# Kernel tuning notes

Hardware: AMD Instinct MI355X
Metric: run time of the kernel (lower is better)

The kernel has to match this reference:

```python
import jax, jax.numpy as jnp
import numpy as np

IN_DIMS = [3, 16, 16]
OUT_DIMS = [16, 16, 3]
GRID_SIZE = 8
SPLINE_ORDER = 3
GRID_RANGE = (-1.0, 1.0)
K = GRID_SIZE + SPLINE_ORDER  # number of B-spline basis functions = 11

# extended knot grid, identical for every feature (as in standard KAN layers)
_h = (GRID_RANGE[1] - GRID_RANGE[0]) / GRID_SIZE
GRID_NP = np.arange(-SPLINE_ORDER, GRID_SIZE + SPLINE_ORDER + 1, dtype=np.float32) * _h + GRID_RANGE[0]

# per-layer parameter slice boundaries: [coef, univariate_weight, residual_weight] per layer
_sizes = [0]
for di, do in zip(IN_DIMS, OUT_DIMS):
    _sizes.extend([di * do * K, di * do, di * do])
PARAM_IDX = np.cumsum(_sizes)
KAN_PARAMS_NUM = int(PARAM_IDX[-1])  # 4576


def bspline_basis(x, grid):
    """Cox-de Boor recursion. x: [...,], grid: [G]. Returns [..., K]."""
    x = x[..., None]
    b = ((x >= grid[:-1]) & (x < grid[1:])).astype(x.dtype)
    for p in range(1, SPLINE_ORDER + 1):
        left = (x - grid[:-(p + 1)]) / (grid[p:-1] - grid[:-(p + 1)]) * b[..., :-1]
        right = (grid[p + 1:] - x) / (grid[p + 1:] - grid[1:-p]) * b[..., 1:]
        b = left + right
    return b  # [..., GRID_SIZE + SPLINE_ORDER]


def setup_inputs() -> dict:
    key = jax.random.key(0)
    k1, k2, k3, k4 = jax.random.split(key, 4)
    B, C, H, W = 8, 3, 224, 224
    x = jax.random.uniform(k1, (B, C, H, W), dtype=jnp.float32)  # in grid range
    features = jax.random.normal(k2, (B, 1000), dtype=jnp.float32)  # resnet18 output stand-in
    fc_w = jax.random.normal(k3, (KAN_PARAMS_NUM, 1000), dtype=jnp.float32) * 0.02
    fc_b = jax.random.normal(k4, (KAN_PARAMS_NUM,), dtype=jnp.float32) * 0.02
    return {"x": x, "features": features, "fc_w": fc_w, "fc_b": fc_b}


def reference(x, features, fc_w, fc_b):
    B, C, H, W = x.shape
    # hypernetwork head: per-sample flat KAN parameter vector [B, P]
    w = features @ fc_w.T + fc_b
    # image -> per-pixel tokens [B, T, C]
    y = jnp.transpose(x, (0, 2, 3, 1)).reshape(B, H * W, C)
    grid = jnp.asarray(GRID_NP, dtype=x.dtype)
    for n, (di, do) in enumerate(zip(IN_DIMS, OUT_DIMS)):
        i0, i1, i2, i3 = PARAM_IDX[3 * n: 3 * n + 4]
        coef = w[:, i0:i1].reshape(B, di, do, K)       # spline coefficients
        uw = w[:, i1:i2].reshape(B, di, do)            # univariate (spline) weight
        rw = w[:, i2:i3].reshape(B, di, do)            # residual (silu) weight
        basis = bspline_basis(y, grid)                 # [B, T, di, K]
        spline = jnp.einsum('btik,biok->bto', basis, coef * uw[..., None])
        base = jnp.einsum('bti,bio->bto', jax.nn.silu(y), rw)
        y = spline + base                              # [B, T, do]
    out = y.reshape(B, H, W, -1)
    return jnp.transpose(out, (0, 3, 1, 2))
```

## Files before the change

### kernel.cpp

```cpp
#include <hip/hip_runtime.h>

#define HW   50176
#define NPAR 4576

typedef _Float16 half8 __attribute__((ext_vector_type(8)));
typedef __attribute__((ext_vector_type(4))) float f32x4;
typedef __attribute__((ext_vector_type(4))) int int4v;

__device__ __forceinline__ unsigned short f2h(float f) {
    union { _Float16 h; unsigned short u; } c; c.h = (_Float16)f; return c.u;
}
__device__ __forceinline__ float h2f(unsigned short u) {
    union { _Float16 h; unsigned short u; } c; c.u = u; return (float)c.h;
}

__global__ __launch_bounds__(256) void gemm_w(const float* __restrict__ feats,
                                              const float* __restrict__ fcw,
                                              const float* __restrict__ fcb,
                                              float* __restrict__ wout) {
    __shared__ float red[4][64][4];
    int tid = threadIdx.x, lane = tid & 63, wave = tid >> 6;
    int nn = lane & 15, quad = lane >> 4;
    int n = blockIdx.x * 16 + nn;
    const float* brow = fcw + (size_t)n * 1000;
    const float* arow = feats + nn * 1000;

    f32x4 acc = {0.f, 0.f, 0.f, 0.f};
#pragma unroll 4
    for (int s8 = 0; s8 < 8; s8++) {
        int kb = (wave * 8 + s8) * 32 + quad * 8;
        float4 a0 = {0,0,0,0}, a1 = {0,0,0,0}, b0 = {0,0,0,0}, b1 = {0,0,0,0};
        if (kb < 1000) {
            b0 = *(const float4*)(brow + kb);
            b1 = *(const float4*)(brow + kb + 4);
            if (nn < 8) {
                a0 = *(const float4*)(arow + kb);
                a1 = *(const float4*)(arow + kb + 4);
            }
        }
        float af[8] = {a0.x, a0.y, a0.z, a0.w, a1.x, a1.y, a1.z, a1.w};
        float bf[8] = {b0.x, b0.y, b0.z, b0.w, b1.x, b1.y, b1.z, b1.w};
        half8 ah, al, bh;
#pragma unroll
        for (int j = 0; j < 8; j++) {
            ah[j] = (_Float16)af[j];
            al[j] = (_Float16)(af[j] - (float)ah[j]);
            bh[j] = (_Float16)bf[j];
        }
        acc = __builtin_amdgcn_mfma_f32_16x16x32_f16(ah, bh, acc, 0, 0, 0);
        acc = __builtin_amdgcn_mfma_f32_16x16x32_f16(al, bh, acc, 0, 0, 0);
    }
#pragma unroll
    for (int r = 0; r < 4; r++) red[wave][lane][r] = acc[r];
    __syncthreads();
    if (wave == 0 && quad < 2) {
        float bias = fcb[n];
#pragma unroll
        for (int r = 0; r < 4; r++) {
            float v = red[0][lane][r] + red[1][lane][r]
                    + red[2][lane][r] + red[3][lane][r];
            wout[(size_t)(quad * 4 + r) * NPAR + n] = v + bias;
        }
    }
}

__global__ __launch_bounds__(256) void pack_b(const float* __restrict__ w,
                                              unsigned int* __restrict__ bt) {
    int idx = blockIdx.x * 256 + threadIdx.x;
    if (idx >= 8 * 4608) return;
    int b = idx / 4608, r = idx - b * 4608;
    int ks = r >> 8, ln = (r >> 2) & 63, dq = r & 3;
    int q = ln >> 4, n = ln & 15;
    int lay, s;
    if (ks < 2)       { lay = 0; s = ks; }
    else if (ks < 10) { lay = 1; s = ks - 2; }
    else              { lay = 2; s = ks - 10; }
    int i = 2 * s + (q >> 1);
    const float* wb = w + b * NPAR;
    int cb, ub, rb2, nd, ni;
    if (lay == 0)      { cb = 0;    ub = 528;  rb2 = 576;  nd = 16; ni = 3;  }
    else if (lay == 1) { cb = 624;  ub = 3440; rb2 = 3696; nd = 16; ni = 16; }
    else               { cb = 3952; ub = 4480; rb2 = 4528; nd = 3;  ni = 16; }
    unsigned int pk = 0;
    if (i < ni && n < nd) {
        float uwv = wb[ub + i * nd + n];
        float rwv = wb[rb2 + i * nd + n];
        unsigned short rh = f2h(rwv);
        float rl = rwv - h2f(rh);
#pragma unroll
        for (int h = 0; h < 2; h++) {
            int rk = (q & 1) * 8 + dq * 2 + h;
            float v = 0.f;
            if (rk < 11)       v = wb[cb + (i * nd + n) * 11 + rk] * uwv;
            else if (rk < 13)  v = rwv;
            else if (rk == 13) v = rl;
            pk |= ((unsigned int)f2h(v)) << (16 * h);
        }
    }
    bt[idx] = pk;
}

__device__ __forceinline__ void scatter_row(int* g0, int* g1, float y) {
    float t  = (y + 1.75f) * 4.0f;
    float ft = floorf(t);
    ft = fminf(fmaxf(ft, -8.0f), 24.0f);
    int jt  = (int)ft;
    float u = t - ft;
    float u2 = u * u, u3 = u2 * u, om = 1.0f - u;
    float b0 = (1.0f / 6.0f) * om * om * om;
    float b3 = (1.0f / 6.0f) * u3;
    float b1 = 0.5f * u3 - u2 + (2.0f / 3.0f);
    float b2 = 1.0f - b0 - b1 - b3;
    float sil = y / (1.0f + __expf(-y));
    unsigned short sh = f2h(sil);
    float sl = sil - h2f(sh);
    int4v z = {0, 0, 0, 0};
    int4v w1;
    w1[0] = 0;
    w1[1] = (int)((unsigned int)sh << 16);
    w1[2] = (int)((unsigned int)f2h(sl) | ((unsigned int)sh << 16));
    w1[3] = 0;
    *(int4v*)g0 = z;
    *(int4v*)g1 = w1;
    int r0 = jt - 3;
    unsigned short hb[4] = {f2h(b0), f2h(b1), f2h(b2), f2h(b3)};
#pragma unroll
    for (int j = 0; j < 4; j++) {
        int s = r0 + j;
        int slot = ((unsigned)s <= 10u) ? s : 15;
        short* sp = (short*)((slot < 8) ? g0 : g1);
        sp[slot & 7] = (short)hb[j];
    }
}

#define YBOFF 1024

__global__ __launch_bounds__(64) void kan_mfma(const float* __restrict__ x,
                                               const unsigned int* __restrict__ bt,
                                               float* __restrict__ out) {
    __shared__ __align__(16) int lds[YBOFF + 64 * 17];
    const int lane = threadIdx.x;
    const int quad = lane >> 4, nn = lane & 15;
    const int b = blockIdx.x / 784;
    const int px0 = (blockIdx.x - b * 784) * 64;
    const unsigned int* btb = bt + b * 4608;
    float* ybf = (float*)&lds[YBOFF];

    int* gp[4];
#pragma unroll
    for (int g = 0; g < 4; g++)
        gp[g] = &lds[lane * 16 + ((((lane >> 1) + g) & 3) * 4)];

    const int aob = nn * 16 + (((nn >> 1) + quad) & 3) * 4;

    const float* xg = x + (size_t)b * 3 * HW + px0 + lane;
    float xv0 = xg[0], xv1 = xg[HW], xv2 = xg[2 * HW];

    f32x4 acc[4];

    auto kstep = [&](int ks) {
        union { half8 h; int4v v; } bf;
        bf.v = *(const int4v*)(btb + ks * 256 + lane * 4);
        asm volatile("s_waitcnt lgkmcnt(0)" ::: "memory");
#pragma unroll
        for (int mt = 0; mt < 4; mt++) {
            union { half8 h; int4v v; } af;
            af.v = *(int4v*)&lds[aob + mt * 256];
            acc[mt] = __builtin_amdgcn_mfma_f32_16x16x32_f16(af.h, bf.h, acc[mt], 0, 0, 0);
        }
    };

#pragma unroll
    for (int mt = 0; mt < 4; mt++) acc[mt] = (f32x4){0.f, 0.f, 0.f, 0.f};
    scatter_row(gp[0], gp[1], xv0);
    scatter_row(gp[2], gp[3], xv1);
    kstep(0);
    asm volatile("" ::: "memory");
    scatter_row(gp[0], gp[1], xv2);
    kstep(1);
#pragma unroll
    for (int mt = 0; mt < 4; mt++)
#pragma unroll
        for (int r = 0; r < 4; r++)
            ybf[(mt * 16 + quad * 4 + r) * 17 + nn] = acc[mt][r];
    asm volatile("s_waitcnt lgkmcnt(0)" ::: "memory");

#pragma unroll
    for (int mt = 0; mt < 4; mt++) acc[mt] = (f32x4){0.f, 0.f, 0.f, 0.f};
#pragma unroll 1
    for (int s = 0; s < 8; s++) {
        float y0 = ybf[lane * 17 + 2 * s];
        float y1 = ybf[lane * 17 + 2 * s + 1];
        asm volatile("" ::: "memory");
        scatter_row(gp[0], gp[1], y0);
        scatter_row(gp[2], gp[3], y1);
        kstep(2 + s);
    }
#pragma unroll
    for (int mt = 0; mt < 4; mt++)
#pragma unroll
        for (int r = 0; r < 4; r++)
            ybf[(mt * 16 + quad * 4 + r) * 17 + nn] = acc[mt][r];
    asm volatile("s_waitcnt lgkmcnt(0)" ::: "memory");

#pragma unroll
    for (int mt = 0; mt < 4; mt++) acc[mt] = (f32x4){0.f, 0.f, 0.f, 0.f};
#pragma unroll 1
    for (int s = 0; s < 8; s++) {
        float y0 = ybf[lane * 17 + 2 * s];
        float y1 = ybf[lane * 17 + 2 * s + 1];
        asm volatile("" ::: "memory");
        scatter_row(gp[0], gp[1], y0);
        scatter_row(gp[2], gp[3], y1);
        kstep(10 + s);
    }

    if (nn < 3) {
#pragma unroll
        for (int mt = 0; mt < 4; mt++)
#pragma unroll
            for (int r = 0; r < 4; r++)
                ybf[(mt * 16 + quad * 4 + r) * 17 + nn] = acc[mt][r];
    }
    asm volatile("s_waitcnt lgkmcnt(0)" ::: "memory");
    float c0 = ybf[lane * 17 + 0];
    float c1 = ybf[lane * 17 + 1];
    float c2 = ybf[lane * 17 + 2];
    float* ob = out + (size_t)b * 3 * HW + px0 + lane;
    ob[0]      = c0;
    ob[HW]     = c1;
    ob[2 * HW] = c2;
}

extern "C" void kernel_launch(void* const* d_in, const int* in_sizes, int n_in,
                              void* d_out, int out_size, void* d_ws, size_t ws_size,
                              hipStream_t stream) {
    const float* x     = (const float*)d_in[0];
    const float* feats = (const float*)d_in[1];
    const float* fcw   = (const float*)d_in[2];
    const float* fcb   = (const float*)d_in[3];
    float* outp = (float*)d_out;
    float* wbuf = (float*)d_ws;
    unsigned int* btens = (unsigned int*)d_ws + 36608;

    hipLaunchKernelGGL(gemm_w, dim3(286), dim3(256), 0, stream,
                       feats, fcw, fcb, wbuf);
    hipLaunchKernelGGL(pack_b, dim3(144), dim3(256), 0, stream,
                       wbuf, btens);
    hipLaunchKernelGGL(kan_mfma, dim3(8 * 784), dim3(64), 0, stream,
                       x, btens, outp);
}
```

Measured before the change: 114.4 us.

## Pad LDS A-tile rows, preload layer activations into registers, cheaper silu/pack

Replaces the XOR-swizzled 16-int LDS rows with padded stride-20 rows so each pixel's A row is contiguous, which simplifies the scatter address math and is meant to avoid bank conflicts. The intermediate activations are preloaded into registers with float2 LDS reads once per layer instead of two scalar reads per iteration. Silu now uses a hardware reciprocal, and the residual split is packed with cvt_pkrtz. The change adds register pressure and slightly more LDS, uses round-toward-zero for the low half, and adds a clamp on the spline fraction.

```diff
diff --git a/kernel.cpp b/kernel.cpp
--- a/kernel.cpp
+++ b/kernel.cpp
@@ -4,6 +4,7 @@
 #define NPAR 4576
 
 typedef _Float16 half8 __attribute__((ext_vector_type(8)));
+typedef __fp16 fp16x2 __attribute__((ext_vector_type(2)));
 typedef __attribute__((ext_vector_type(4))) float f32x4;
 typedef __attribute__((ext_vector_type(4))) int int4v;
 
@@ -100,45 +101,52 @@
     bt[idx] = pk;
 }
 
-__device__ __forceinline__ void scatter_row(int* g0, int* g1, float y) {
+__device__ __forceinline__ void scatter_row(int* rowp, float y) {
     float t  = (y + 1.75f) * 4.0f;
     float ft = floorf(t);
     ft = fminf(fmaxf(ft, -8.0f), 24.0f);
-    int jt  = (int)ft;
     float u = t - ft;
+    u = fminf(fmaxf(u, -8.0f), 8.0f);
     float u2 = u * u, u3 = u2 * u, om = 1.0f - u;
     float b0 = (1.0f / 6.0f) * om * om * om;
     float b3 = (1.0f / 6.0f) * u3;
     float b1 = 0.5f * u3 - u2 + (2.0f / 3.0f);
     float b2 = 1.0f - b0 - b1 - b3;
-    float sil = y / (1.0f + __expf(-y));
+    float sil = y * __builtin_amdgcn_rcpf(1.0f + __expf(-y));
+
     unsigned short sh = f2h(sil);
     float sl = sil - h2f(sh);
+    union { fp16x2 h; int i; } pk;
+    pk.h = __builtin_amdgcn_cvt_pkrtz(sl, sil);
+
     int4v z = {0, 0, 0, 0};
     int4v w1;
     w1[0] = 0;
     w1[1] = (int)((unsigned int)sh << 16);
-    w1[2] = (int)((unsigned int)f2h(sl) | ((unsigned int)sh << 16));
+    w1[2] = pk.i;
     w1[3] = 0;
-    *(int4v*)g0 = z;
-    *(int4v*)g1 = w1;
-    int r0 = jt - 3;
+    *(int4v*)rowp = z;
+    *(int4v*)(rowp + 4) = w1;
+
+    int jt3 = (int)ft - 3;
+    short* sp = (short*)rowp;
     unsigned short hb[4] = {f2h(b0), f2h(b1), f2h(b2), f2h(b3)};
 #pragma unroll
     for (int j = 0; j < 4; j++) {
-        int s = r0 + j;
+        int s = jt3 + j;
         int slot = ((unsigned)s <= 10u) ? s : 15;
-        short* sp = (short*)((slot < 8) ? g0 : g1);
-        sp[slot & 7] = (short)hb[j];
-    }
-}
-
-#define YBOFF 1024
+        sp[slot] = (short)hb[j];
+    }
+}
+
+#define ASTR  20
+#define YSTR  18
+#define YBOFF (64 * ASTR)
 
 __global__ __launch_bounds__(64) void kan_mfma(const float* __restrict__ x,
                                                const unsigned int* __restrict__ bt,
                                                float* __restrict__ out) {
-    __shared__ __align__(16) int lds[YBOFF + 64 * 17];
+    __shared__ __align__(16) int lds[YBOFF + 64 * YSTR];
     const int lane = threadIdx.x;
     const int quad = lane >> 4, nn = lane & 15;
     const int b = blockIdx.x / 784;
@@ -146,12 +154,9 @@
     const unsigned int* btb = bt + b * 4608;
     float* ybf = (float*)&lds[YBOFF];
 
-    int* gp[4];
-#pragma unroll
-    for (int g = 0; g < 4; g++)
-        gp[g] = &lds[lane * 16 + ((((lane >> 1) + g) & 3) * 4)];
-
-    const int aob = nn * 16 + (((nn >> 1) + quad) & 3) * 4;
+    int* rowE = &lds[ASTR * lane];
+    int* rowO = rowE + 8;
+    const int aob = ASTR * nn + 4 * quad;
 
     const float* xg = x + (size_t)b * 3 * HW + px0 + lane;
     float xv0 = xg[0], xv1 = xg[HW], xv2 = xg[2 * HW];
@@ -165,54 +170,66 @@
 #pragma unroll
         for (int mt = 0; mt < 4; mt++) {
             union { half8 h; int4v v; } af;
-            af.v = *(int4v*)&lds[aob + mt * 256];
+            af.v = *(int4v*)&lds[aob + mt * (16 * ASTR)];
             acc[mt] = __builtin_amdgcn_mfma_f32_16x16x32_f16(af.h, bf.h, acc[mt], 0, 0, 0);
         }
     };
 
 #pragma unroll
     for (int mt = 0; mt < 4; mt++) acc[mt] = (f32x4){0.f, 0.f, 0.f, 0.f};
-    scatter_row(gp[0], gp[1], xv0);
-    scatter_row(gp[2], gp[3], xv1);
+    scatter_row(rowE, xv0);
+    scatter_row(rowO, xv1);
     kstep(0);
     asm volatile("" ::: "memory");
-    scatter_row(gp[0], gp[1], xv2);
+    scatter_row(rowE, xv2);
     kstep(1);
 #pragma unroll
     for (int mt = 0; mt < 4; mt++)
 #pragma unroll
         for (int r = 0; r < 4; r++)
-            ybf[(mt * 16 + quad * 4 + r) * 17 + nn] = acc[mt][r];
+            ybf[(mt * 16 + quad * 4 + r) * YSTR + nn] = acc[mt][r];
     asm volatile("s_waitcnt lgkmcnt(0)" ::: "memory");
 
-#pragma unroll
-    for (int mt = 0; mt < 4; mt++) acc[mt] = (f32x4){0.f, 0.f, 0.f, 0.f};
+    {
+        float yv[16];
+#pragma unroll
+        for (int j = 0; j < 8; j++) {
+            float2 p = *(const float2*)&ybf[lane * YSTR + 2 * j];
+            yv[2 * j] = p.x; yv[2 * j + 1] = p.y;
+        }
+#pragma unroll
+        for (int mt = 0; mt < 4; mt++) acc[mt] = (f32x4){0.f, 0.f, 0.f, 0.f};
 #pragma unroll 1
-    for (int s = 0; s < 8; s++) {
-        float y0 = ybf[lane * 17 + 2 * s];
-        float y1 = ybf[lane * 17 + 2 * s + 1];
-        asm volatile("" ::: "memory");
-        scatter_row(gp[0], gp[1], y0);
-        scatter_row(gp[2], gp[3], y1);
-        kstep(2 + s);
+        for (int s = 0; s < 8; s++) {
+            asm volatile("" ::: "memory");
+            scatter_row(rowE, yv[2 * s]);
+            scatter_row(rowO, yv[2 * s + 1]);
+            kstep(2 + s);
+        }
     }
 #pragma unroll
     for (int mt = 0; mt < 4; mt++)
 #pragma unroll
         for (int r = 0; r < 4; r++)
-            ybf[(mt * 16 + quad * 4 + r) * 17 + nn] = acc[mt][r];
+            ybf[(mt * 16 + quad * 4 + r) * YSTR + nn] = acc[mt][r];
     asm volatile("s_waitcnt lgkmcnt(0)" ::: "memory");
 
-#pragma unroll
-    for (int mt = 0; mt < 4; mt++) acc[mt] = (f32x4){0.f, 0.f, 0.f, 0.f};
+    {
+        float yv[16];
+#pragma unroll
+        for (int j = 0; j < 8; j++) {
+            float2 p = *(const float2*)&ybf[lane * YSTR + 2 * j];
+            yv[2 * j] = p.x; yv[2 * j + 1] = p.y;
+        }
+#pragma unroll
+        for (int mt = 0; mt < 4; mt++) acc[mt] = (f32x4){0.f, 0.f, 0.f, 0.f};
 #pragma unroll 1
-    for (int s = 0; s < 8; s++) {
-        float y0 = ybf[lane * 17 + 2 * s];
-        float y1 = ybf[lane * 17 + 2 * s + 1];
-        asm volatile("" ::: "memory");
-        scatter_row(gp[0], gp[1], y0);
-        scatter_row(gp[2], gp[3], y1);
-        kstep(10 + s);
+        for (int s = 0; s < 8; s++) {
+            asm volatile("" ::: "memory");
+            scatter_row(rowE, yv[2 * s]);
+            scatter_row(rowO, yv[2 * s + 1]);
+            kstep(10 + s);
+        }
     }
 
     if (nn < 3) {
@@ -220,12 +237,12 @@
         for (int mt = 0; mt < 4; mt++)
 #pragma unroll
             for (int r = 0; r < 4; r++)
-                ybf[(mt * 16 + quad * 4 + r) * 17 + nn] = acc[mt][r];
+                ybf[(mt * 16 + quad * 4 + r) * YSTR + nn] = acc[mt][r];
     }
     asm volatile("s_waitcnt lgkmcnt(0)" ::: "memory");
-    float c0 = ybf[lane * 17 + 0];
-    float c1 = ybf[lane * 17 + 1];
-    float c2 = ybf[lane * 17 + 2];
+    float c0 = ybf[lane * YSTR + 0];
+    float c1 = ybf[lane * YSTR + 1];
+    float c2 = ybf[lane * YSTR + 2];
     float* ob = out + (size_t)b * 3 * HW + px0 + lane;
     ob[0]      = c0;
     ob[HW]     = c1;
```

New measurement: 114.0 us. About the same (-0.4%).
